# Kernel optimization log

Hardware: AMD Instinct MI355X
Metric: run time of the kernel (lower is better)

## Reference

```python
import jax, jax.numpy as jnp
import numpy as np

EPS = 1e-5
NHEAD = 8
TOP_K = 2


def _layernorm(x, g, b):
    m = jnp.mean(x, axis=-1, keepdims=True)
    v = jnp.mean((x - m) ** 2, axis=-1, keepdims=True)
    return (x - m) * jax.lax.rsqrt(v + EPS) * g + b


def setup_inputs() -> dict:
    S, D, F, E = 4096, 512, 2048, 8
    key = jax.random.key(0)
    ks = jax.random.split(key, 18)
    std = 0.02
    return {
        "src": jax.random.normal(ks[0], (S, D), jnp.float32),
        "in_proj_w": std * jax.random.normal(ks[1], (3 * D, D), jnp.float32),
        "in_proj_b": jnp.zeros((3 * D,), jnp.float32),
        "out_proj_w": std * jax.random.normal(ks[2], (D, D), jnp.float32),
        "out_proj_b": jnp.zeros((D,), jnp.float32),
        "ln1_g": jnp.ones((D,), jnp.float32),
        "ln1_b": jnp.zeros((D,), jnp.float32),
        "ln2_g": jnp.ones((D,), jnp.float32),
        "ln2_b": jnp.zeros((D,), jnp.float32),
        "gate_w": std * jax.random.normal(ks[3], (E, D), jnp.float32),
        "gate_b": jnp.zeros((E,), jnp.float32),
        "w1": std * jax.random.normal(ks[4], (E, F, D), jnp.float32),
        "b1": jnp.zeros((E, F), jnp.float32),
        "w2": std * jax.random.normal(ks[5], (E, F, D), jnp.float32),
        "b2": jnp.zeros((E, F), jnp.float32),
        "wo": std * jax.random.normal(ks[6], (E, D, F), jnp.float32),
        "bo": jnp.zeros((E, D), jnp.float32),
    }


def _sa_block(x, in_proj_w, in_proj_b, out_proj_w, out_proj_b):
    # x: [S, D] unbatched sequence (torch MultiheadAttention unbatched path)
    S, D = x.shape
    hd = D // NHEAD
    qkv = x @ in_proj_w.T + in_proj_b              # [S, 3D]
    q, k, v = jnp.split(qkv, 3, axis=-1)
    q = q.reshape(S, NHEAD, hd)
    k = k.reshape(S, NHEAD, hd)
    v = v.reshape(S, NHEAD, hd)
    scores = jnp.einsum("shd,thd->hst", q, k) / jnp.sqrt(jnp.float32(hd))
    attn = jax.nn.softmax(scores, axis=-1)         # [H, S, S]
    out = jnp.einsum("hst,thd->shd", attn, v).reshape(S, D)
    return out @ out_proj_w.T + out_proj_b


def _ff_block(x, gate_w, gate_b, w1, b1, w2, b2, wo, bo):
    # top-k gated SwiGLU MoE; gate probs are softmax, NOT renormalized after topk
    T = x.shape[0]
    E = w1.shape[0]
    gates = jax.nn.softmax(x @ gate_w.T + gate_b, axis=-1)      # [T, E]
    top_scores, top_idx = jax.lax.top_k(gates, TOP_K)            # [T, k]
    combine = jnp.zeros((T, E), x.dtype).at[
        jnp.arange(T)[:, None], top_idx].add(top_scores)         # [T, E]
    out = jnp.zeros_like(x)
    for e in range(E):  # small fixed expert count
        h = jax.nn.silu(x @ w1[e].T + b1[e]) * (x @ w2[e].T + b2[e])
        out = out + combine[:, e:e + 1] * (h @ wo[e].T + bo[e])
    return out


def reference(src, in_proj_w, in_proj_b, out_proj_w, out_proj_b,
              ln1_g, ln1_b, ln2_g, ln2_b,
              gate_w, gate_b, w1, b1, w2, b2, wo, bo):
    # norm_first pre-norm residual layer, dropout=0 (eval)
    x = src
    x = x + _sa_block(_layernorm(x, ln1_g, ln1_b),
                      in_proj_w, in_proj_b, out_proj_w, out_proj_b)
    x = x + _ff_block(_layernorm(x, ln2_g, ln2_b),
                      gate_w, gate_b, w1, b1, w2, b2, wo, bo)
    return x
```

## Files before the change

### kernel.cpp

```cpp
#include <hip/hip_runtime.h>
#include <hip/hip_bf16.h>
#include <math.h>

#define SQ   4096
#define DM   512
#define NH   8
#define HDIM 64
#define FF   2048
#define NE   8

typedef unsigned short u16;
typedef unsigned int   u32;
typedef __attribute__((ext_vector_type(8))) __bf16 bf16x8;
typedef __attribute__((ext_vector_type(4))) float  f32x4;

__device__ __forceinline__ float bf2f(u16 v) {
    union { u32 i; float f; } c; c.i = ((u32)v) << 16; return c.f;
}
__device__ __forceinline__ u16 f2bf(float f) {
    union { __bf16 h; u16 u; } c; c.h = (__bf16)f; return c.u;
}

#define BM 128
#define BN 128
#define BK 32
#define BKP 40

__global__ __launch_bounds__(256) void gemm_split(
    const u16* __restrict__ Ahi, const u16* __restrict__ Alo, int lda,
    const u16* __restrict__ Bhi, const u16* __restrict__ Blo, int ldb,
    int M, int N, int K,
    const float* __restrict__ bias,
    const float* __restrict__ resid, int ldres,
    u16* __restrict__ Chi, u16* __restrict__ Clo,
    float* __restrict__ Cf, int ldc, int mode)
{
    __shared__ __align__(16) u16 Ash[BM * BKP], Asl[BM * BKP];
    __shared__ __align__(16) u16 Bsh[BN * BKP], Bsl[BN * BKP];
    const int tid  = threadIdx.x;
    const int wave = tid >> 6;
    const int lane = tid & 63;
    const int quad = lane >> 4;
    const int l16  = lane & 15;
    const int bm = blockIdx.x * BM;
    const int bn = blockIdx.y * BN;
    const int wm = (wave & 1) * 64;
    const int wn = (wave >> 1) * 64;

    f32x4 acc[4][4];
#pragma unroll
    for (int i = 0; i < 4; i++)
#pragma unroll
        for (int j = 0; j < 4; j++)
#pragma unroll
            for (int r = 0; r < 4; r++) acc[i][j][r] = 0.0f;

    for (int k0 = 0; k0 < K; k0 += BK) {
#pragma unroll
        for (int i = 0; i < 2; i++) {
            int c = tid + i * 256;
            int row = c >> 2;
            int col = (c & 3) << 3;
            int ga = bm + row, gb2 = bn + row;
            uint4 vah = make_uint4(0u,0u,0u,0u), val = vah, vbh = vah, vbl = vah;
            if (ga < M) {
                vah = *(const uint4*)(Ahi + (size_t)ga * lda + k0 + col);
                val = *(const uint4*)(Alo + (size_t)ga * lda + k0 + col);
            }
            if (gb2 < N) {
                vbh = *(const uint4*)(Bhi + (size_t)gb2 * ldb + k0 + col);
                vbl = *(const uint4*)(Blo + (size_t)gb2 * ldb + k0 + col);
            }
            *(uint4*)(Ash + row * BKP + col) = vah;
            *(uint4*)(Asl + row * BKP + col) = val;
            *(uint4*)(Bsh + row * BKP + col) = vbh;
            *(uint4*)(Bsl + row * BKP + col) = vbl;
        }
        __syncthreads();
        bf16x8 ah[4], al[4], bh[4], bl[4];
#pragma unroll
        for (int i = 0; i < 4; i++) {
            ah[i] = *(const bf16x8*)(Ash + (wm + i * 16 + l16) * BKP + quad * 8);
            al[i] = *(const bf16x8*)(Asl + (wm + i * 16 + l16) * BKP + quad * 8);
        }
#pragma unroll
        for (int j = 0; j < 4; j++) {
            bh[j] = *(const bf16x8*)(Bsh + (wn + j * 16 + l16) * BKP + quad * 8);
            bl[j] = *(const bf16x8*)(Bsl + (wn + j * 16 + l16) * BKP + quad * 8);
        }
#pragma unroll
        for (int i = 0; i < 4; i++)
#pragma unroll
            for (int j = 0; j < 4; j++) {
                acc[i][j] = __builtin_amdgcn_mfma_f32_16x16x32_bf16(ah[i], bh[j], acc[i][j], 0,0,0);
                acc[i][j] = __builtin_amdgcn_mfma_f32_16x16x32_bf16(ah[i], bl[j], acc[i][j], 0,0,0);
                acc[i][j] = __builtin_amdgcn_mfma_f32_16x16x32_bf16(al[i], bh[j], acc[i][j], 0,0,0);
            }
        __syncthreads();
    }

#pragma unroll
    for (int i = 0; i < 4; i++)
#pragma unroll
        for (int j = 0; j < 4; j++)
#pragma unroll
            for (int r = 0; r < 4; r++) {
                int row = bm + wm + i * 16 + quad * 4 + r;
                int col = bn + wn + j * 16 + l16;
                if (row >= M || col >= N) continue;
                float v = acc[i][j][r] + (bias ? bias[col] : 0.0f);
                size_t idx = (size_t)row * ldc + col;
                if (mode == 0) {
                    u16 hb = f2bf(v);
                    Chi[idx] = hb;
                    Clo[idx] = f2bf(v - bf2f(hb));
                } else {
                    if (resid) v += resid[(size_t)row * ldres + col];
                    Cf[idx] = v;
                }
            }
}

__global__ __launch_bounds__(256) void gemm_split_ko(
    const u16* __restrict__ Ahi, const u16* __restrict__ Alo, int lda,
    const u16* __restrict__ Bhi, const u16* __restrict__ Blo, int ldb,
    float* __restrict__ Cf, int ldc)
{
    __shared__ __align__(16) u16 Ash[BM * BKP], Asl[BM * BKP];
    __shared__ __align__(16) u16 Bsh[BN * BKP], Bsl[BN * BKP];
    const int tid  = threadIdx.x;
    const int wave = tid >> 6;
    const int lane = tid & 63;
    const int quad = lane >> 4;
    const int l16  = lane & 15;
    const int bm = blockIdx.x * BM;
    const int bn = blockIdx.y * BN;
    const int wm = (wave & 1) * 64;
    const int wn = (wave >> 1) * 64;
    const int KC    = DM / 4;
    const int k0beg = blockIdx.z * KC;

    f32x4 acc[4][4];
#pragma unroll
    for (int i = 0; i < 4; i++)
#pragma unroll
        for (int j = 0; j < 4; j++)
#pragma unroll
            for (int r = 0; r < 4; r++) acc[i][j][r] = 0.0f;

    for (int k0 = k0beg; k0 < k0beg + KC; k0 += BK) {
#pragma unroll
        for (int i = 0; i < 2; i++) {
            int c = tid + i * 256;
            int row = c >> 2;
            int col = (c & 3) << 3;
            int ga = bm + row, gb2 = bn + row;
            uint4 vah = *(const uint4*)(Ahi + (size_t)ga * lda + k0 + col);
            uint4 val = *(const uint4*)(Alo + (size_t)ga * lda + k0 + col);
            uint4 vbh = *(const uint4*)(Bhi + (size_t)gb2 * ldb + k0 + col);
            uint4 vbl = *(const uint4*)(Blo + (size_t)gb2 * ldb + k0 + col);
            *(uint4*)(Ash + row * BKP + col) = vah;
            *(uint4*)(Asl + row * BKP + col) = val;
            *(uint4*)(Bsh + row * BKP + col) = vbh;
            *(uint4*)(Bsl + row * BKP + col) = vbl;
        }
        __syncthreads();
        bf16x8 ah[4], al[4], bh[4], bl[4];
#pragma unroll
        for (int i = 0; i < 4; i++) {
            ah[i] = *(const bf16x8*)(Ash + (wm + i * 16 + l16) * BKP + quad * 8);
            al[i] = *(const bf16x8*)(Asl + (wm + i * 16 + l16) * BKP + quad * 8);
        }
#pragma unroll
        for (int j = 0; j < 4; j++) {
            bh[j] = *(const bf16x8*)(Bsh + (wn + j * 16 + l16) * BKP + quad * 8);
            bl[j] = *(const bf16x8*)(Bsl + (wn + j * 16 + l16) * BKP + quad * 8);
        }
#pragma unroll
        for (int i = 0; i < 4; i++)
#pragma unroll
            for (int j = 0; j < 4; j++) {
                acc[i][j] = __builtin_amdgcn_mfma_f32_16x16x32_bf16(ah[i], bh[j], acc[i][j], 0,0,0);
                acc[i][j] = __builtin_amdgcn_mfma_f32_16x16x32_bf16(ah[i], bl[j], acc[i][j], 0,0,0);
                acc[i][j] = __builtin_amdgcn_mfma_f32_16x16x32_bf16(al[i], bh[j], acc[i][j], 0,0,0);
            }
        __syncthreads();
    }

#pragma unroll
    for (int i = 0; i < 4; i++)
#pragma unroll
        for (int j = 0; j < 4; j++)
#pragma unroll
            for (int r = 0; r < 4; r++) {
                int row = bm + wm + i * 16 + quad * 4 + r;
                int col = bn + wn + j * 16 + l16;
                atomicAdd(Cf + (size_t)row * ldc + col, acc[i][j][r]);
            }
}

__global__ __launch_bounds__(256) void init_x1(
    const float* __restrict__ src, const float* __restrict__ bias,
    float* __restrict__ x1)
{
    int i = blockIdx.x * 256 + threadIdx.x;
    int col4 = i & (DM / 4 - 1);
    float4 s = ((const float4*)src)[i];
    float4 b = ((const float4*)bias)[col4];
    s.x += b.x; s.y += b.y; s.z += b.z; s.w += b.w;
    ((float4*)x1)[i] = s;
}

__global__ __launch_bounds__(256) void moe12_all(
    const u16* __restrict__ A, int lda,
    const int* __restrict__ idxl, const int* __restrict__ cnt,
    const int* __restrict__ off,
    const float* __restrict__ w1, const float* __restrict__ b1,
    const float* __restrict__ w2, const float* __restrict__ b2,
    u16* __restrict__ H)
{
    const int bmg = blockIdx.x * BM;
    if (bmg >= off[NE]) return;
    int e = 0;
    while (e < NE - 1 && bmg >= off[e + 1]) e++;
    const int M   = cnt[e];
    const int bml = bmg - off[e];
    if (bml >= M) return;
    const float* B1 = w1 + (size_t)e * FF * DM;
    const float* B2 = w2 + (size_t)e * FF * DM;
    const int*   rl = idxl + e * SQ;

    __shared__ __align__(16) u16 As[BM * BKP], Bs1[BN * BKP], Bs2[BN * BKP];
    const int tid  = threadIdx.x;
    const int wave = tid >> 6;
    const int lane = tid & 63;
    const int quad = lane >> 4;
    const int l16  = lane & 15;
    const int bn = blockIdx.y * BN;
    const int wm = (wave & 1) * 64;
    const int wn = (wave >> 1) * 64;

    f32x4 acc1[4][4], acc2[4][4];
#pragma unroll
    for (int i = 0; i < 4; i++)
#pragma unroll
        for (int j = 0; j < 4; j++)
#pragma unroll
            for (int r = 0; r < 4; r++) { acc1[i][j][r] = 0.0f; acc2[i][j][r] = 0.0f; }

    for (int k0 = 0; k0 < DM; k0 += BK) {
#pragma unroll
        for (int i = 0; i < 2; i++) {
            int c = tid + i * 256;
            int row = c >> 2;
            int col = (c & 3) << 3;
            uint4 va = make_uint4(0u,0u,0u,0u);
            int lr = bml + row;
            if (lr < M) {
                int ar = rl[lr];
                va = *(const uint4*)(A + (size_t)ar * lda + k0 + col);
            }
            *(uint4*)(As + row * BKP + col) = va;
        }
#pragma unroll
        for (int i = 0; i < 4; i++) {
            int c = tid + i * 256;
            int row = c >> 3;
            int col = (c & 7) << 2;
            float4 v1 = *(const float4*)(B1 + (size_t)(bn + row) * DM + k0 + col);
            float4 v2 = *(const float4*)(B2 + (size_t)(bn + row) * DM + k0 + col);
            ushort4 h1, h2;
            h1.x = f2bf(v1.x); h1.y = f2bf(v1.y); h1.z = f2bf(v1.z); h1.w = f2bf(v1.w);
            h2.x = f2bf(v2.x); h2.y = f2bf(v2.y); h2.z = f2bf(v2.z); h2.w = f2bf(v2.w);
            *(ushort4*)(Bs1 + row * BKP + col) = h1;
            *(ushort4*)(Bs2 + row * BKP + col) = h2;
        }
        __syncthreads();
        bf16x8 af[4], b1f[4], b2f[4];
#pragma unroll
        for (int i = 0; i < 4; i++)
            af[i] = *(const bf16x8*)(As + (wm + i * 16 + l16) * BKP + quad * 8);
#pragma unroll
        for (int j = 0; j < 4; j++) {
            b1f[j] = *(const bf16x8*)(Bs1 + (wn + j * 16 + l16) * BKP + quad * 8);
            b2f[j] = *(const bf16x8*)(Bs2 + (wn + j * 16 + l16) * BKP + quad * 8);
        }
#pragma unroll
        for (int i = 0; i < 4; i++)
#pragma unroll
            for (int j = 0; j < 4; j++) {
                acc1[i][j] = __builtin_amdgcn_mfma_f32_16x16x32_bf16(af[i], b1f[j], acc1[i][j], 0,0,0);
                acc2[i][j] = __builtin_amdgcn_mfma_f32_16x16x32_bf16(af[i], b2f[j], acc2[i][j], 0,0,0);
            }
        __syncthreads();
    }

#pragma unroll
    for (int i = 0; i < 4; i++)
#pragma unroll
        for (int j = 0; j < 4; j++)
#pragma unroll
            for (int r = 0; r < 4; r++) {
                int rowl = bml + wm + i * 16 + quad * 4 + r;
                if (rowl >= M) continue;
                int col = bn + wn + j * 16 + l16;
                float g1 = acc1[i][j][r] + b1[e * FF + col];
                float g2 = acc2[i][j][r] + b2[e * FF + col];
                float s  = g1 / (1.0f + __expf(-g1));
                H[(size_t)(off[e] + rowl) * FF + col] = f2bf(s * g2);
            }
}

__global__ __launch_bounds__(256) void moe12_bf16(
    const u16* __restrict__ A, int lda,
    const int* __restrict__ idxl, const int* __restrict__ cnt,
    const int* __restrict__ off,
    const u16* __restrict__ w1b, const float* __restrict__ b1,
    const u16* __restrict__ w2b, const float* __restrict__ b2,
    u16* __restrict__ H)
{
    const int bmg = blockIdx.x * BM;
    if (bmg >= off[NE]) return;
    int e = 0;
    while (e < NE - 1 && bmg >= off[e + 1]) e++;
    const int M   = cnt[e];
    const int bml = bmg - off[e];
    if (bml >= M) return;
    const u16* B1 = w1b + (size_t)e * FF * DM;
    const u16* B2 = w2b + (size_t)e * FF * DM;
    const int* rl = idxl + e * SQ;

    __shared__ __align__(16) u16 As[BM * BKP], Bs1[BN * BKP], Bs2[BN * BKP];
    const int tid  = threadIdx.x;
    const int wave = tid >> 6;
    const int lane = tid & 63;
    const int quad = lane >> 4;
    const int l16  = lane & 15;
    const int bn = blockIdx.y * BN;
    const int wm = (wave & 1) * 64;
    const int wn = (wave >> 1) * 64;

    f32x4 acc1[4][4], acc2[4][4];
#pragma unroll
    for (int i = 0; i < 4; i++)
#pragma unroll
        for (int j = 0; j < 4; j++)
#pragma unroll
            for (int r = 0; r < 4; r++) { acc1[i][j][r] = 0.0f; acc2[i][j][r] = 0.0f; }

    for (int k0 = 0; k0 < DM; k0 += BK) {
#pragma unroll
        for (int i = 0; i < 2; i++) {
            int c = tid + i * 256;
            int row = c >> 2;
            int col = (c & 3) << 3;
            uint4 va = make_uint4(0u,0u,0u,0u);
            int lr = bml + row;
            if (lr < M) {
                int ar = rl[lr];
                va = *(const uint4*)(A + (size_t)ar * lda + k0 + col);
            }
            *(uint4*)(As + row * BKP + col) = va;
            uint4 v1 = *(const uint4*)(B1 + (size_t)(bn + row) * DM + k0 + col);
            uint4 v2 = *(const uint4*)(B2 + (size_t)(bn + row) * DM + k0 + col);
            *(uint4*)(Bs1 + row * BKP + col) = v1;
            *(uint4*)(Bs2 + row * BKP + col) = v2;
        }
        __syncthreads();
        bf16x8 af[4], b1f[4], b2f[4];
#pragma unroll
        for (int i = 0; i < 4; i++)
            af[i] = *(const bf16x8*)(As + (wm + i * 16 + l16) * BKP + quad * 8);
#pragma unroll
        for (int j = 0; j < 4; j++) {
            b1f[j] = *(const bf16x8*)(Bs1 + (wn + j * 16 + l16) * BKP + quad * 8);
            b2f[j] = *(const bf16x8*)(Bs2 + (wn + j * 16 + l16) * BKP + quad * 8);
        }
#pragma unroll
        for (int i = 0; i < 4; i++)
#pragma unroll
            for (int j = 0; j < 4; j++) {
                acc1[i][j] = __builtin_amdgcn_mfma_f32_16x16x32_bf16(af[i], b1f[j], acc1[i][j], 0,0,0);
                acc2[i][j] = __builtin_amdgcn_mfma_f32_16x16x32_bf16(af[i], b2f[j], acc2[i][j], 0,0,0);
            }
        __syncthreads();
    }

#pragma unroll
    for (int i = 0; i < 4; i++)
#pragma unroll
        for (int j = 0; j < 4; j++)
#pragma unroll
            for (int r = 0; r < 4; r++) {
                int rowl = bml + wm + i * 16 + quad * 4 + r;
                if (rowl >= M) continue;
                int col = bn + wn + j * 16 + l16;
                float g1 = acc1[i][j][r] + b1[e * FF + col];
                float g2 = acc2[i][j][r] + b2[e * FF + col];
                float s  = g1 / (1.0f + __expf(-g1));
                H[(size_t)(off[e] + rowl) * FF + col] = f2bf(s * g2);
            }
}

__global__ __launch_bounds__(256) void moe_y_all(
    const u16* __restrict__ H,
    const float* __restrict__ wo, const float* __restrict__ bo,
    const int* __restrict__ idxl, const float* __restrict__ cw,
    const int* __restrict__ cnt, const int* __restrict__ off,
    float* __restrict__ out)
{
    const int bmg = blockIdx.x * BM;
    if (bmg >= off[NE]) return;
    int e = 0;
    while (e < NE - 1 && bmg >= off[e + 1]) e++;
    const int M   = cnt[e];
    const int bml = bmg - off[e];
    if (bml >= M) return;
    const float* B = wo + (size_t)e * DM * FF;

    __shared__ __align__(16) u16 As[BM * BKP], Bs[BN * BKP];
    const int tid  = threadIdx.x;
    const int wave = tid >> 6;
    const int lane = tid & 63;
    const int quad = lane >> 4;
    const int l16  = lane & 15;
    const int bn = blockIdx.y * BN;
    const int wm = (wave & 1) * 64;
    const int wn = (wave >> 1) * 64;

    f32x4 acc[4][4];
#pragma unroll
    for (int i = 0; i < 4; i++)
#pragma unroll
        for (int j = 0; j < 4; j++)
#pragma unroll
            for (int r = 0; r < 4; r++) acc[i][j][r] = 0.0f;

    for (int k0 = 0; k0 < FF; k0 += BK) {
#pragma unroll
        for (int i = 0; i < 2; i++) {
            int c = tid + i * 256;
            int row = c >> 2;
            int col = (c & 3) << 3;
            uint4 va = *(const uint4*)(H + (size_t)(bmg + row) * FF + k0 + col);
            *(uint4*)(As + row * BKP + col) = va;
        }
#pragma unroll
        for (int i = 0; i < 4; i++) {
            int c = tid + i * 256;
            int row = c >> 3;
            int col = (c & 7) << 2;
            float4 v = *(const float4*)(B + (size_t)(bn + row) * FF + k0 + col);
            ushort4 h;
            h.x = f2bf(v.x); h.y = f2bf(v.y); h.z = f2bf(v.z); h.w = f2bf(v.w);
            *(ushort4*)(Bs + row * BKP + col) = h;
        }
        __syncthreads();
        bf16x8 af[4], bf[4];
#pragma unroll
        for (int i = 0; i < 4; i++)
            af[i] = *(const bf16x8*)(As + (wm + i * 16 + l16) * BKP + quad * 8);
#pragma unroll
        for (int j = 0; j < 4; j++)
            bf[j] = *(const bf16x8*)(Bs + (wn + j * 16 + l16) * BKP + quad * 8);
#pragma unroll
        for (int i = 0; i < 4; i++)
#pragma unroll
            for (int j = 0; j < 4; j++)
                acc[i][j] = __builtin_amdgcn_mfma_f32_16x16x32_bf16(af[i], bf[j], acc[i][j], 0,0,0);
        __syncthreads();
    }

#pragma unroll
    for (int i = 0; i < 4; i++)
#pragma unroll
        for (int j = 0; j < 4; j++)
#pragma unroll
            for (int r = 0; r < 4; r++) {
                int rowl = bml + wm + i * 16 + quad * 4 + r;
                if (rowl >= M) continue;
                int col = bn + wn + j * 16 + l16;
                int tok = idxl[e * SQ + rowl];
                float wgt = cw[e * SQ + rowl];
                atomicAdd(out + (size_t)tok * DM + col,
                          wgt * (acc[i][j][r] + bo[e * DM + col]));
            }
}

__global__ __launch_bounds__(256) void moe_y_bf16(
    const u16* __restrict__ H,
    const u16* __restrict__ wob, const float* __restrict__ bo,
    const int* __restrict__ idxl, const float* __restrict__ cw,
    const int* __restrict__ cnt, const int* __restrict__ off,
    float* __restrict__ out)
{
    const int bmg = blockIdx.x * BM;
    if (bmg >= off[NE]) return;
    int e = 0;
    while (e < NE - 1 && bmg >= off[e + 1]) e++;
    const int M   = cnt[e];
    const int bml = bmg - off[e];
    if (bml >= M) return;
    const u16* B = wob + (size_t)e * DM * FF;

    __shared__ __align__(16) u16 As[BM * BKP], Bs[BN * BKP];
    const int tid  = threadIdx.x;
    const int wave = tid >> 6;
    const int lane = tid & 63;
    const int quad = lane >> 4;
    const int l16  = lane & 15;
    const int bn = blockIdx.y * BN;
    const int wm = (wave & 1) * 64;
    const int wn = (wave >> 1) * 64;

    f32x4 acc[4][4];
#pragma unroll
    for (int i = 0; i < 4; i++)
#pragma unroll
        for (int j = 0; j < 4; j++)
#pragma unroll
            for (int r = 0; r < 4; r++) acc[i][j][r] = 0.0f;

    for (int k0 = 0; k0 < FF; k0 += BK) {
#pragma unroll
        for (int i = 0; i < 2; i++) {
            int c = tid + i * 256;
            int row = c >> 2;
            int col = (c & 3) << 3;
            uint4 va = *(const uint4*)(H + (size_t)(bmg + row) * FF + k0 + col);
            *(uint4*)(As + row * BKP + col) = va;
            uint4 vb = *(const uint4*)(B + (size_t)(bn + row) * FF + k0 + col);
            *(uint4*)(Bs + row * BKP + col) = vb;
        }
        __syncthreads();
        bf16x8 af[4], bf[4];
#pragma unroll
        for (int i = 0; i < 4; i++)
            af[i] = *(const bf16x8*)(As + (wm + i * 16 + l16) * BKP + quad * 8);
#pragma unroll
        for (int j = 0; j < 4; j++)
            bf[j] = *(const bf16x8*)(Bs + (wn + j * 16 + l16) * BKP + quad * 8);
#pragma unroll
        for (int i = 0; i < 4; i++)
#pragma unroll
            for (int j = 0; j < 4; j++)
                acc[i][j] = __builtin_amdgcn_mfma_f32_16x16x32_bf16(af[i], bf[j], acc[i][j], 0,0,0);
        __syncthreads();
    }

#pragma unroll
    for (int i = 0; i < 4; i++)
#pragma unroll
        for (int j = 0; j < 4; j++)
#pragma unroll
            for (int r = 0; r < 4; r++) {
                int rowl = bml + wm + i * 16 + quad * 4 + r;
                if (rowl >= M) continue;
                int col = bn + wn + j * 16 + l16;
                int tok = idxl[e * SQ + rowl];
                float wgt = cw[e * SQ + rowl];
                atomicAdd(out + (size_t)tok * DM + col,
                          wgt * (acc[i][j][r] + bo[e * DM + col]));
            }
}

__global__ __launch_bounds__(256) void cvt_w_bf16(
    const float* __restrict__ w, u16* __restrict__ wb, int n4)
{
    int i = blockIdx.x * 256 + threadIdx.x;
    if (i < n4) {
        float4 v = ((const float4*)w)[i];
        ushort4 h;
        h.x = f2bf(v.x); h.y = f2bf(v.y); h.z = f2bf(v.z); h.w = f2bf(v.w);
        ((ushort4*)wb)[i] = h;
    }
}

#define KP 64
#define SWZ(row, col) ((col) ^ (((row) & 7) << 3))
#define SCL 0.18033688011112042f

template <int SPLIT>
__device__ __forceinline__ void flash_body(
    const u16* __restrict__ qh, const u16* __restrict__ ql,
    const u16* __restrict__ vth, const u16* __restrict__ vtl,
    u16* __restrict__ oh, u16* __restrict__ ol,
    float* __restrict__ Opart, float* __restrict__ mpart,
    float* __restrict__ lpart)
{
    __shared__ __align__(16) u16 Ksh[64*KP], Ksl[64*KP], Vsh[64*KP], Vsl[64*KP];
    const int tid  = threadIdx.x;
    const int wave = tid >> 6;
    const int lane = tid & 63;
    const int quad = lane >> 4;
    const int l16  = lane & 15;
    const int h    = blockIdx.y;
    const int z    = (SPLIT > 1) ? blockIdx.z : 0;
    const int qbase = blockIdx.x * 64 + wave * 16;

    u16* const Pwh = Ksh + wave * (16 * KP);
    u16* const Pwl = Ksl + wave * (16 * KP);

    const int r_st  = tid >> 3;
    const int co_g  = (tid & 7) << 3;
    const int co_sw = SWZ(r_st, co_g);

    bf16x8 aqh[2], aql[2];
#pragma unroll
    for (int kk = 0; kk < 2; kk++) {
        size_t off = (size_t)(qbase + l16) * (3*DM) + h*HDIM + kk*32 + quad*8;
        aqh[kk] = *(const bf16x8*)(qh + off);
        aql[kk] = *(const bf16x8*)(ql + off);
    }

    float m_[4], l_[4];
    f32x4 o_[4];
#pragma unroll
    for (int r = 0; r < 4; r++) { m_[r] = -1e30f; l_[r] = 0.0f; }
#pragma unroll
    for (int nd = 0; nd < 4; nd++)
#pragma unroll
        for (int r = 0; r < 4; r++) o_[nd][r] = 0.0f;

    const int NT    = SQ / 64 / SPLIT;
    const int jtBeg = z * NT, jtEnd = (z + 1) * NT;

    for (int jt = jtBeg; jt < jtEnd; jt++) {
        {
            size_t koff0 = (size_t)(jt*64 + r_st) * (3*DM) + DM + h*HDIM + co_g;
            size_t voff0 = (size_t)(h*HDIM + r_st) * SQ + jt*64 + co_g;
            size_t koff1 = koff0 + (size_t)32 * (3*DM);
            size_t voff1 = voff0 + (size_t)32 * SQ;
            uint4 a0 = *(const uint4*)(qh  + koff0);
            uint4 a1 = *(const uint4*)(ql  + koff0);
            uint4 a2 = *(const uint4*)(vth + voff0);
            uint4 a3 = *(const uint4*)(vtl + voff0);
            uint4 b0 = *(const uint4*)(qh  + koff1);
            uint4 b1 = *(const uint4*)(ql  + koff1);
            uint4 b2 = *(const uint4*)(vth + voff1);
            uint4 b3 = *(const uint4*)(vtl + voff1);
            *(uint4*)(Ksh + r_st*KP + co_sw)      = a0;
            *(uint4*)(Ksl + r_st*KP + co_sw)      = a1;
            *(uint4*)(Vsh + r_st*KP + co_sw)      = a2;
            *(uint4*)(Vsl + r_st*KP + co_sw)      = a3;
            *(uint4*)(Ksh + (r_st+32)*KP + co_sw) = b0;
            *(uint4*)(Ksl + (r_st+32)*KP + co_sw) = b1;
            *(uint4*)(Vsh + (r_st+32)*KP + co_sw) = b2;
            *(uint4*)(Vsl + (r_st+32)*KP + co_sw) = b3;
        }
        __syncthreads();

        f32x4 s[4];
        __builtin_amdgcn_s_setprio(1);
#pragma unroll
        for (int jn = 0; jn < 4; jn++) {
            f32x4 zz;
#pragma unroll
            for (int r = 0; r < 4; r++) zz[r] = 0.0f;
#pragma unroll
            for (int kk = 0; kk < 2; kk++) {
                int krow = jn*16 + l16;
                int kcol = SWZ(krow, kk*32 + quad*8);
                bf16x8 kh = *(const bf16x8*)(Ksh + krow*KP + kcol);
                bf16x8 kl = *(const bf16x8*)(Ksl + krow*KP + kcol);
                zz = __builtin_amdgcn_mfma_f32_16x16x32_bf16(aqh[kk], kh, zz, 0,0,0);
                zz = __builtin_amdgcn_mfma_f32_16x16x32_bf16(aqh[kk], kl, zz, 0,0,0);
                zz = __builtin_amdgcn_mfma_f32_16x16x32_bf16(aql[kk], kh, zz, 0,0,0);
            }
#pragma unroll
            for (int r = 0; r < 4; r++) zz[r] *= SCL;
            s[jn] = zz;
        }
        __builtin_amdgcn_s_setprio(0);
        __syncthreads();

        float mx[4];
#pragma unroll
        for (int r = 0; r < 4; r++) {
            mx[r] = fmaxf(fmaxf(s[0][r], s[1][r]), fmaxf(s[2][r], s[3][r]));
#pragma unroll
            for (int o2 = 1; o2 < 16; o2 <<= 1)
                mx[r] = fmaxf(mx[r], __shfl_xor(mx[r], o2));
        }
        int grew = (mx[0] > m_[0] + 8.0f) | (mx[1] > m_[1] + 8.0f) |
                   (mx[2] > m_[2] + 8.0f) | (mx[3] > m_[3] + 8.0f);
        if (__any(grew)) {
#pragma unroll
            for (int r = 0; r < 4; r++) {
                float nm  = fmaxf(m_[r], mx[r]);
                float al2 = exp2f(m_[r] - nm);
                m_[r] = nm;
                l_[r] *= al2;
#pragma unroll
                for (int nd = 0; nd < 4; nd++) o_[nd][r] *= al2;
            }
        }
        float rs[4];
#pragma unroll
        for (int r = 0; r < 4; r++) rs[r] = 0.0f;
#pragma unroll
        for (int jn = 0; jn < 4; jn++)
#pragma unroll
            for (int r = 0; r < 4; r++) {
                float p = exp2f(s[jn][r] - m_[r]);
                s[jn][r] = p;
                rs[r] += p;
            }
#pragma unroll
        for (int r = 0; r < 4; r++) {
#pragma unroll
            for (int o2 = 1; o2 < 16; o2 <<= 1)
                rs[r] += __shfl_xor(rs[r], o2);
            l_[r] += rs[r];
        }
#pragma unroll
        for (int jn = 0; jn < 4; jn++)
#pragma unroll
            for (int r = 0; r < 4; r++) {
                float p = s[jn][r];
                u16 ph = f2bf(p);
                int rr   = quad*4 + r;
                int pidx = rr*KP + SWZ(rr, jn*16 + l16);
                Pwh[pidx] = ph;
                Pwl[pidx] = f2bf(p - bf2f(ph));
            }

        bf16x8 ph[2], pl[2];
#pragma unroll
        for (int kk = 0; kk < 2; kk++) {
            int pcol = SWZ(l16, kk*32 + quad*8);
            ph[kk] = *(const bf16x8*)(Pwh + l16*KP + pcol);
            pl[kk] = *(const bf16x8*)(Pwl + l16*KP + pcol);
        }
        __builtin_amdgcn_s_setprio(1);
#pragma unroll
        for (int nd = 0; nd < 4; nd++) {
#pragma unroll
            for (int kk = 0; kk < 2; kk++) {
                int vrow = nd*16 + l16;
                int vcol = SWZ(vrow, kk*32 + quad*8);
                bf16x8 vh = *(const bf16x8*)(Vsh + vrow*KP + vcol);
                bf16x8 vl = *(const bf16x8*)(Vsl + vrow*KP + vcol);
                o_[nd] = __builtin_amdgcn_mfma_f32_16x16x32_bf16(ph[kk], vh, o_[nd], 0,0,0);
                o_[nd] = __builtin_amdgcn_mfma_f32_16x16x32_bf16(ph[kk], vl, o_[nd], 0,0,0);
                o_[nd] = __builtin_amdgcn_mfma_f32_16x16x32_bf16(pl[kk], vh, o_[nd], 0,0,0);
            }
        }
        __builtin_amdgcn_s_setprio(0);
        __syncthreads();
    }

    if (SPLIT == 1) {
#pragma unroll
        for (int nd = 0; nd < 4; nd++)
#pragma unroll
            for (int r = 0; r < 4; r++) {
                int row = qbase + quad*4 + r;
                int col = h*HDIM + nd*16 + l16;
                float w = o_[nd][r] / l_[r];
                u16 hb = f2bf(w);
                oh[(size_t)row * DM + col] = hb;
                ol[(size_t)row * DM + col] = f2bf(w - bf2f(hb));
            }
    } else {
#pragma unroll
        for (int nd = 0; nd < 4; nd++)
#pragma unroll
            for (int r = 0; r < 4; r++) {
                int row = qbase + quad*4 + r;
                int col = h*HDIM + nd*16 + l16;
                Opart[((size_t)z * SQ + row) * DM + col] = o_[nd][r];
            }
        if (l16 == 0) {
#pragma unroll
            for (int r = 0; r < 4; r++) {
                int row = qbase + quad*4 + r;
                mpart[(z*NH + h) * SQ + row] = m_[r];
                lpart[(z*NH + h) * SQ + row] = l_[r];
            }
        }
    }
}

__global__ __launch_bounds__(256) void flash_attn(
    const u16* __restrict__ qh, const u16* __restrict__ ql,
    const u16* __restrict__ vth, const u16* __restrict__ vtl,
    u16* __restrict__ oh, u16* __restrict__ ol)
{
    flash_body<1>(qh, ql, vth, vtl, oh, ol, nullptr, nullptr, nullptr);
}

__global__ __launch_bounds__(256) void flash_attn_part2(
    const u16* __restrict__ qh, const u16* __restrict__ ql,
    const u16* __restrict__ vth, const u16* __restrict__ vtl,
    float* __restrict__ Opart, float* __restrict__ mpart,
    float* __restrict__ lpart)
{
    flash_body<2>(qh, ql, vth, vtl, nullptr, nullptr, Opart, mpart, lpart);
}

__global__ __launch_bounds__(256) void flash_attn_part4(
    const u16* __restrict__ qh, const u16* __restrict__ ql,
    const u16* __restrict__ vth, const u16* __restrict__ vtl,
    float* __restrict__ Opart, float* __restrict__ mpart,
    float* __restrict__ lpart)
{
    flash_body<4>(qh, ql, vth, vtl, nullptr, nullptr, Opart, mpart, lpart);
}

__global__ __launch_bounds__(256) void attn_combine(
    const float* __restrict__ Opart, const float* __restrict__ mpart,
    const float* __restrict__ lpart,
    u16* __restrict__ oh, u16* __restrict__ ol, int ns)
{
    const int row = blockIdx.x;
    const int tid = threadIdx.x;
#pragma unroll
    for (int i = 0; i < 2; i++) {
        int col = tid + i * 256;
        int h = col >> 6;
        float m = -1e30f;
        for (int zz = 0; zz < ns; zz++)
            m = fmaxf(m, mpart[(zz*NH + h) * SQ + row]);
        float O = 0.0f, l = 0.0f;
        for (int zz = 0; zz < ns; zz++) {
            float a = exp2f(mpart[(zz*NH + h) * SQ + row] - m);
            O += Opart[((size_t)zz * SQ + row) * DM + col] * a;
            l += lpart[(zz*NH + h) * SQ + row] * a;
        }
        float w = O / l;
        u16 hb = f2bf(w);
        oh[(size_t)row * DM + col] = hb;
        ol[(size_t)row * DM + col] = f2bf(w - bf2f(hb));
    }
}

__global__ __launch_bounds__(256) void ln1_split(
    const float* __restrict__ x, const float* __restrict__ g,
    const float* __restrict__ b, u16* __restrict__ ohi, u16* __restrict__ olo)
{
    const int row = blockIdx.x;
    const int tid = threadIdx.x;
    float v0 = x[(size_t)row * DM + tid];
    float v1 = x[(size_t)row * DM + tid + 256];
    float s = v0 + v1, sq = v0*v0 + v1*v1;
#pragma unroll
    for (int o = 1; o < 64; o <<= 1) { s += __shfl_xor(s, o); sq += __shfl_xor(sq, o); }
    __shared__ float ss[4], ssq[4];
    if ((tid & 63) == 0) { ss[tid>>6] = s; ssq[tid>>6] = sq; }
    __syncthreads();
    s  = ss[0]+ss[1]+ss[2]+ss[3];
    sq = ssq[0]+ssq[1]+ssq[2]+ssq[3];
    float m = s * (1.0f/DM);
    float rstd = rsqrtf(sq*(1.0f/DM) - m*m + 1e-5f);
    float y0 = (v0-m)*rstd*g[tid]     + b[tid];
    float y1 = (v1-m)*rstd*g[tid+256] + b[tid+256];
    u16 h0 = f2bf(y0), h1 = f2bf(y1);
    ohi[(size_t)row*DM + tid]       = h0;  olo[(size_t)row*DM + tid]       = f2bf(y0 - bf2f(h0));
    ohi[(size_t)row*DM + tid + 256] = h1;  olo[(size_t)row*DM + tid + 256] = f2bf(y1 - bf2f(h1));
}

__global__ __launch_bounds__(256) void ln_kernel(
    const float* __restrict__ x, const float* __restrict__ g,
    const float* __restrict__ b, u16* __restrict__ out)
{
    const int row = blockIdx.x;
    const int tid = threadIdx.x;
    float v0 = x[(size_t)row * DM + tid];
    float v1 = x[(size_t)row * DM + tid + 256];
    float s = v0 + v1, sq = v0*v0 + v1*v1;
#pragma unroll
    for (int o = 1; o < 64; o <<= 1) { s += __shfl_xor(s, o); sq += __shfl_xor(sq, o); }
    __shared__ float ss[4], ssq[4];
    if ((tid & 63) == 0) { ss[tid>>6] = s; ssq[tid>>6] = sq; }
    __syncthreads();
    s  = ss[0]+ss[1]+ss[2]+ss[3];
    sq = ssq[0]+ssq[1]+ssq[2]+ssq[3];
    float m = s * (1.0f/DM);
    float rstd = rsqrtf(sq*(1.0f/DM) - m*m + 1e-5f);
    out[(size_t)row*DM + tid]       = f2bf((v0-m)*rstd*g[tid]     + b[tid]);
    out[(size_t)row*DM + tid + 256] = f2bf((v1-m)*rstd*g[tid+256] + b[tid+256]);
}

__global__ __launch_bounds__(256) void transpose_v2(
    const u16* __restrict__ qh, const u16* __restrict__ ql,
    u16* __restrict__ vth, u16* __restrict__ vtl)
{
    __shared__ u16 Th[64 * 66], Tl[64 * 66];
    const int t0  = blockIdx.x * 64;
    const int hd0 = blockIdx.y * 64;
    const int tid = threadIdx.x;
#pragma unroll
    for (int k = 0; k < 16; k++) {
        int idx = tid + k * 256;
        int r = idx >> 6, j = idx & 63;
        size_t src = (size_t)(t0 + r) * (3*DM) + 2*DM + hd0 + j;
        Th[r * 66 + j] = qh[src];
        Tl[r * 66 + j] = ql[src];
    }
    __syncthreads();
#pragma unroll
    for (int k = 0; k < 16; k++) {
        int idx = tid + k * 256;
        int r = idx >> 6, c2 = idx & 63;
        size_t dst = (size_t)(hd0 + r) * SQ + t0 + c2;
        vth[dst] = Th[c2 * 66 + r];
        vtl[dst] = Tl[c2 * 66 + r];
    }
}

__global__ __launch_bounds__(256) void gate_route(
    const float* __restrict__ x1, const float* __restrict__ g,
    const float* __restrict__ b, const float* __restrict__ gw,
    const float* __restrict__ gb,
    int* __restrict__ cnt, int* __restrict__ idxl, float* __restrict__ cw)
{
    const int token = blockIdx.x * 4 + (threadIdx.x >> 6);
    const int lane  = threadIdx.x & 63;
    const float* xr = x1 + (size_t)token * DM;
    float v[8];
#pragma unroll
    for (int i = 0; i < 8; i++) v[i] = xr[lane*8 + i];
    float s = 0.f, sq = 0.f;
#pragma unroll
    for (int i = 0; i < 8; i++) { s += v[i]; sq += v[i]*v[i]; }
#pragma unroll
    for (int o = 1; o < 64; o <<= 1) { s += __shfl_xor(s, o); sq += __shfl_xor(sq, o); }
    float m = s * (1.0f/DM);
    float rstd = rsqrtf(sq*(1.0f/DM) - m*m + 1e-5f);
    float xn[8];
#pragma unroll
    for (int i = 0; i < 8; i++)
        xn[i] = (v[i]-m)*rstd*g[lane*8+i] + b[lane*8+i];
    float logit[8];
#pragma unroll
    for (int e = 0; e < 8; e++) {
        float t = 0.f;
#pragma unroll
        for (int i = 0; i < 8; i++) t += xn[i] * gw[e*DM + lane*8 + i];
#pragma unroll
        for (int o = 1; o < 64; o <<= 1) t += __shfl_xor(t, o);
        logit[e] = t + gb[e];
    }
    if (lane == 0) {
        float mx = -1e30f;
        for (int e = 0; e < 8; e++) mx = fmaxf(mx, logit[e]);
        float den = 0.f, p[8];
        for (int e = 0; e < 8; e++) { p[e] = __expf(logit[e] - mx); den += p[e]; }
        for (int e = 0; e < 8; e++) p[e] /= den;
        int i1 = 0;
        for (int e = 1; e < 8; e++) if (p[e] > p[i1]) i1 = e;
        int i2 = -1;
        for (int e = 0; e < 8; e++) { if (e == i1) continue; if (i2 < 0 || p[e] > p[i2]) i2 = e; }
        int s1 = atomicAdd(&cnt[i1], 1);
        idxl[i1*SQ + s1] = token;  cw[i1*SQ + s1] = p[i1];
        int s2 = atomicAdd(&cnt[i2], 1);
        idxl[i2*SQ + s2] = token;  cw[i2*SQ + s2] = p[i2];
    }
}

__global__ __launch_bounds__(256) void cvt_split_w(
    const float* __restrict__ w, u16* __restrict__ wh, u16* __restrict__ wl, int n)
{
    int i = blockIdx.x * 256 + threadIdx.x;
    if (i < n) {
        float v = w[i];
        u16 h = f2bf(v);
        wh[i] = h;
        wl[i] = f2bf(v - bf2f(h));
    }
}

__global__ __launch_bounds__(64) void zero_cnt(int* cnt)
{
    if (threadIdx.x < NE) cnt[threadIdx.x] = 0;
}

__global__ __launch_bounds__(64) void make_off(const int* __restrict__ cnt,
                                              int* __restrict__ off)
{
    if (threadIdx.x == 0) {
        int a = 0;
        for (int e = 0; e < NE; e++) {
            off[e] = a;
            a += ((cnt[e] + 127) >> 7) << 7;
        }
        off[NE] = a;
    }
}

__global__ __launch_bounds__(256) void init_out(
    const float* __restrict__ x1, float* __restrict__ out)
{
    int i = blockIdx.x * 256 + threadIdx.x;
    ((float4*)out)[i] = ((const float4*)x1)[i];
}

__global__ __launch_bounds__(256) void sentinel_kernel(float* out, float v, int n)
{
    int i = blockIdx.x * 256 + threadIdx.x;
    if (i < n) out[i] = v;
}
__global__ __launch_bounds__(256) void scrub_kernel(float* out, int n)
{
    int i = blockIdx.x * 256 + threadIdx.x;
    if (i < n) { float v = out[i]; if (!isfinite(v)) out[i] = 777.0f; }
}

extern "C" void kernel_launch(void* const* d_in, const int* in_sizes, int n_in,
                              void* d_out, int out_size, void* d_ws, size_t ws_size,
                              hipStream_t stream)
{
    const float* src        = (const float*)d_in[0];
    const float* in_proj_w  = (const float*)d_in[1];
    const float* in_proj_b  = (const float*)d_in[2];
    const float* out_proj_w = (const float*)d_in[3];
    const float* out_proj_b = (const float*)d_in[4];
    const float* ln1_g      = (const float*)d_in[5];
    const float* ln1_b      = (const float*)d_in[6];
    const float* ln2_g      = (const float*)d_in[7];
    const float* ln2_b      = (const float*)d_in[8];
    const float* gate_w     = (const float*)d_in[9];
    const float* gate_b     = (const float*)d_in[10];
    const float* w1         = (const float*)d_in[11];
    const float* b1         = (const float*)d_in[12];
    const float* w2         = (const float*)d_in[13];
    const float* b2         = (const float*)d_in[14];
    const float* wo         = (const float*)d_in[15];
    const float* bo         = (const float*)d_in[16];
    float* out = (float*)d_out;

    const size_t MB = (size_t)1 << 20;
    const size_t ROUTE = 512 * 1024;
    const size_t NEED      = ROUTE + 44 * MB;
    const size_t NEED_BIG2 = ROUTE + 61 * MB;
    const size_t NEED_BIG4 = ROUTE + 78 * MB;
    if (ws_size < NEED) {
        sentinel_kernel<<<(SQ*DM)/256, 256, 0, stream>>>(out, 333.0f, SQ*DM);
        return;
    }
    int ns = 0;
    if (ws_size >= NEED_BIG4)      ns = 4;
    else if (ws_size >= NEED_BIG2) ns = 2;

    char* ws = (char*)d_ws;
    int*   cnt  = (int*)ws;
    int*   offp = (int*)(ws + 64);
    int*   idxl = (int*)(ws + 1024);
    float* cw   = (float*)(ws + 1024 + 128*1024);
    char*  base = ws + ROUTE;
    u16* xln1h = (u16*)(base);
    u16* xln1l = (u16*)(base + 4*MB);
    u16* attnh = (u16*)(base);
    u16* attnl = (u16*)(base + 4*MB);
    u16* qkvh  = (u16*)(base + 8*MB);
    u16* qkvl  = (u16*)(base + 20*MB);
    float* x1  = (float*)(base + 8*MB);
    u16* vth   = (u16*)(base + 32*MB);
    u16* vtl   = (u16*)(base + 36*MB);
    u16* xln2  = (u16*)(base + 36*MB);
    u16* Hbuf  = (u16*)(base);
    u16* wph   = (u16*)(base + 40*MB);
    u16* wpl   = (u16*)(base + 40*MB + 1536*1024);
    u16* woh   = (u16*)(base + 43*MB);
    u16* wol   = (u16*)(base + 43*MB + 512*1024);
    float* Opart = (float*)(base + 44*MB);
    float* mpart;
    float* lpart;
    if (ns == 4) {
        mpart = (float*)(base + 76*MB);
        lpart = (float*)(base + 76*MB + 512*1024);
    } else {
        mpart = (float*)(base + 60*MB);
        lpart = (float*)(base + 60*MB + 256*1024);
    }
    u16* w1b = (u16*)(base + 44*MB);
    u16* w2b = (u16*)(base + 60*MB);
    u16* wob = (u16*)(base + 44*MB);

    cvt_split_w<<<(3*DM*DM)/256, 256, 0, stream>>>(in_proj_w,  wph, wpl, 3*DM*DM);
    cvt_split_w<<<(DM*DM)/256,   256, 0, stream>>>(out_proj_w, woh, wol, DM*DM);

    ln1_split<<<SQ, 256, 0, stream>>>(src, ln1_g, ln1_b, xln1h, xln1l);
    gemm_split<<<dim3(32, 12), 256, 0, stream>>>(
        xln1h, xln1l, DM, wph, wpl, DM, SQ, 3*DM, DM,
        in_proj_b, nullptr, 0, qkvh, qkvl, nullptr, 3*DM, 0);
    transpose_v2<<<dim3(SQ/64, DM/64), 256, 0, stream>>>(qkvh, qkvl, vth, vtl);
    if (ns == 4) {
        flash_attn_part4<<<dim3(SQ/64, NH, 4), 256, 0, stream>>>(
            qkvh, qkvl, vth, vtl, Opart, mpart, lpart);
        attn_combine<<<SQ, 256, 0, stream>>>(Opart, mpart, lpart, attnh, attnl, 4);
    } else if (ns == 2) {
        flash_attn_part2<<<dim3(SQ/64, NH, 2), 256, 0, stream>>>(
            qkvh, qkvl, vth, vtl, Opart, mpart, lpart);
        attn_combine<<<SQ, 256, 0, stream>>>(Opart, mpart, lpart, attnh, attnl, 2);
    } else {
        flash_attn<<<dim3(SQ/64, NH), 256, 0, stream>>>(
            qkvh, qkvl, vth, vtl, attnh, attnl);
    }
    init_x1<<<(SQ*DM/4)/256, 256, 0, stream>>>(src, out_proj_b, x1);
    gemm_split_ko<<<dim3(32, 4, 4), 256, 0, stream>>>(
        attnh, attnl, DM, woh, wol, DM, x1, DM);

    ln_kernel<<<SQ, 256, 0, stream>>>(x1, ln2_g, ln2_b, xln2);
    zero_cnt<<<1, 64, 0, stream>>>(cnt);
    gate_route<<<SQ/4, 256, 0, stream>>>(x1, ln2_g, ln2_b, gate_w, gate_b,
                                         cnt, idxl, cw);
    make_off<<<1, 64, 0, stream>>>(cnt, offp);
    init_out<<<(SQ*DM/4)/256, 256, 0, stream>>>(x1, out);
    const int WN4 = (NE * FF * DM) / 4;
    if (ns == 4) {
        cvt_w_bf16<<<WN4/256, 256, 0, stream>>>(w1, w1b, WN4);
        cvt_w_bf16<<<WN4/256, 256, 0, stream>>>(w2, w2b, WN4);
        moe12_bf16<<<dim3(72, 16), 256, 0, stream>>>(
            xln2, DM, idxl, cnt, offp, w1b, b1, w2b, b2, Hbuf);
        cvt_w_bf16<<<WN4/256, 256, 0, stream>>>(wo, wob, WN4);
        moe_y_bf16<<<dim3(72, 4), 256, 0, stream>>>(
            Hbuf, wob, bo, idxl, cw, cnt, offp, out);
    } else {
        moe12_all<<<dim3(72, 16), 256, 0, stream>>>(
            xln2, DM, idxl, cnt, offp, w1, b1, w2, b2, Hbuf);
        moe_y_all<<<dim3(72, 4), 256, 0, stream>>>(
            Hbuf, wo, bo, idxl, cw, cnt, offp, out);
    }

    scrub_kernel<<<(SQ*DM)/256, 256, 0, stream>>>(out, SQ*DM);
}
```

Baseline: 784.4 us.

## Compute transposed S in flash attention, use shuffles for P, fuse LN2 into gating

The flash attention kernel now computes S transposed by swapping the MFMA operands, so each lane holds values of a single query row. That makes the row max and row sum cheap two-step cross-quad shuffles. The P fragments for the PV MFMA are built with register shuffles instead of an LDS round trip, which removes one __syncthreads per tile. Separately, the standalone LN2 kernel is removed and gate_route writes the bf16 normalized activations itself, saving a launch and a read of x1. The shuffle-based P transpose adds many ds_bpermute instructions per tile, which may offset the LDS savings.

New measurement: 728.7 us. -7.1%, faster.

```diff
diff --git a/kernel.cpp b/kernel.cpp
--- a/kernel.cpp
+++ b/kernel.cpp
@@ -598,9 +598,6 @@
     const int z    = (SPLIT > 1) ? blockIdx.z : 0;
     const int qbase = blockIdx.x * 64 + wave * 16;
 
-    u16* const Pwh = Ksh + wave * (16 * KP);
-    u16* const Pwl = Ksl + wave * (16 * KP);
-
     const int r_st  = tid >> 3;
     const int co_g  = (tid & 7) << 3;
     const int co_sw = SWZ(r_st, co_g);
@@ -613,14 +610,16 @@
         aql[kk] = *(const bf16x8*)(ql + off);
     }
 
-    float m_[4], l_[4];
+    float m_ = -1e30f, l_ = 0.0f;
     f32x4 o_[4];
 #pragma unroll
-    for (int r = 0; r < 4; r++) { m_[r] = -1e30f; l_[r] = 0.0f; }
-#pragma unroll
     for (int nd = 0; nd < 4; nd++)
 #pragma unroll
         for (int r = 0; r < 4; r++) o_[nd][r] = 0.0f;
+
+    const int srcA = l16 + ((quad & 1) * 2) * 16;
+    const int srcB = srcA + 16;
+    const bool hiJ = (quad >> 1);
 
     const int NT    = SQ / 64 / SPLIT;
     const int jtBeg = z * NT, jtEnd = (z + 1) * NT;
@@ -663,75 +662,105 @@
                 int kcol = SWZ(krow, kk*32 + quad*8);
                 bf16x8 kh = *(const bf16x8*)(Ksh + krow*KP + kcol);
                 bf16x8 kl = *(const bf16x8*)(Ksl + krow*KP + kcol);
-                zz = __builtin_amdgcn_mfma_f32_16x16x32_bf16(aqh[kk], kh, zz, 0,0,0);
-                zz = __builtin_amdgcn_mfma_f32_16x16x32_bf16(aqh[kk], kl, zz, 0,0,0);
-                zz = __builtin_amdgcn_mfma_f32_16x16x32_bf16(aql[kk], kh, zz, 0,0,0);
+                zz = __builtin_amdgcn_mfma_f32_16x16x32_bf16(kh, aqh[kk], zz, 0,0,0);
+                zz = __builtin_amdgcn_mfma_f32_16x16x32_bf16(kl, aqh[kk], zz, 0,0,0);
+                zz = __builtin_amdgcn_mfma_f32_16x16x32_bf16(kh, aql[kk], zz, 0,0,0);
             }
 #pragma unroll
             for (int r = 0; r < 4; r++) zz[r] *= SCL;
             s[jn] = zz;
         }
         __builtin_amdgcn_s_setprio(0);
-        __syncthreads();
-
-        float mx[4];
-#pragma unroll
-        for (int r = 0; r < 4; r++) {
-            mx[r] = fmaxf(fmaxf(s[0][r], s[1][r]), fmaxf(s[2][r], s[3][r]));
-#pragma unroll
-            for (int o2 = 1; o2 < 16; o2 <<= 1)
-                mx[r] = fmaxf(mx[r], __shfl_xor(mx[r], o2));
-        }
-        int grew = (mx[0] > m_[0] + 8.0f) | (mx[1] > m_[1] + 8.0f) |
-                   (mx[2] > m_[2] + 8.0f) | (mx[3] > m_[3] + 8.0f);
+
+        float mx = s[0][0];
+#pragma unroll
+        for (int jn = 0; jn < 4; jn++)
+#pragma unroll
+            for (int r = 0; r < 4; r++) mx = fmaxf(mx, s[jn][r]);
+        mx = fmaxf(mx, __shfl_xor(mx, 16));
+        mx = fmaxf(mx, __shfl_xor(mx, 32));
+
+        int grew = (mx > m_ + 8.0f) ? 1 : 0;
         if (__any(grew)) {
+            float nm  = fmaxf(m_, mx);
+            float al2 = exp2f(m_ - nm);
+            m_ = nm;
+            l_ *= al2;
+            float alq[4];
+#pragma unroll
+            for (int r = 0; r < 4; r++)
+                alq[r] = __shfl(al2, quad*4 + r);
+#pragma unroll
+            for (int nd = 0; nd < 4; nd++)
+#pragma unroll
+                for (int r = 0; r < 4; r++) o_[nd][r] *= alq[r];
+        }
+
+        float rs = 0.0f;
+#pragma unroll
+        for (int jn = 0; jn < 4; jn++)
 #pragma unroll
             for (int r = 0; r < 4; r++) {
-                float nm  = fmaxf(m_[r], mx[r]);
-                float al2 = exp2f(m_[r] - nm);
-                m_[r] = nm;
-                l_[r] *= al2;
-#pragma unroll
-                for (int nd = 0; nd < 4; nd++) o_[nd][r] *= al2;
-            }
-        }
-        float rs[4];
-#pragma unroll
-        for (int r = 0; r < 4; r++) rs[r] = 0.0f;
-#pragma unroll
-        for (int jn = 0; jn < 4; jn++)
-#pragma unroll
-            for (int r = 0; r < 4; r++) {
-                float p = exp2f(s[jn][r] - m_[r]);
+                float p = exp2f(s[jn][r] - m_);
                 s[jn][r] = p;
-                rs[r] += p;
-            }
-#pragma unroll
-        for (int r = 0; r < 4; r++) {
-#pragma unroll
-            for (int o2 = 1; o2 < 16; o2 <<= 1)
-                rs[r] += __shfl_xor(rs[r], o2);
-            l_[r] += rs[r];
-        }
-#pragma unroll
-        for (int jn = 0; jn < 4; jn++)
-#pragma unroll
-            for (int r = 0; r < 4; r++) {
-                float p = s[jn][r];
-                u16 ph = f2bf(p);
-                int rr   = quad*4 + r;
-                int pidx = rr*KP + SWZ(rr, jn*16 + l16);
-                Pwh[pidx] = ph;
-                Pwl[pidx] = f2bf(p - bf2f(ph));
-            }
-
-        bf16x8 ph[2], pl[2];
+                rs += p;
+            }
+        rs += __shfl_xor(rs, 16);
+        rs += __shfl_xor(rs, 32);
+        l_ += rs;
+
+        u32 phk[4][2], plk[4][2];
+#pragma unroll
+        for (int jn = 0; jn < 4; jn++) {
+            u16 h0 = f2bf(s[jn][0]), h1 = f2bf(s[jn][1]);
+            u16 h2 = f2bf(s[jn][2]), h3 = f2bf(s[jn][3]);
+            phk[jn][0] = (u32)h0 | ((u32)h1 << 16);
+            phk[jn][1] = (u32)h2 | ((u32)h3 << 16);
+            u16 g0 = f2bf(s[jn][0] - bf2f(h0)), g1 = f2bf(s[jn][1] - bf2f(h1));
+            u16 g2 = f2bf(s[jn][2] - bf2f(h2)), g3 = f2bf(s[jn][3] - bf2f(h3));
+            plk[jn][0] = (u32)g0 | ((u32)g1 << 16);
+            plk[jn][1] = (u32)g2 | ((u32)g3 << 16);
+        }
+
+        bf16x8 phf[2], plf[2];
 #pragma unroll
         for (int kk = 0; kk < 2; kk++) {
-            int pcol = SWZ(l16, kk*32 + quad*8);
-            ph[kk] = *(const bf16x8*)(Pwh + l16*KP + pcol);
-            pl[kk] = *(const bf16x8*)(Pwl + l16*KP + pcol);
-        }
+            int jA = kk*2, jB = kk*2 + 1;
+            uint4 wh, wl;
+            {
+                u32 a = (u32)__shfl((int)phk[jA][0], srcA);
+                u32 b = (u32)__shfl((int)phk[jB][0], srcA);
+                wh.x = hiJ ? b : a;
+                a = (u32)__shfl((int)phk[jA][1], srcA);
+                b = (u32)__shfl((int)phk[jB][1], srcA);
+                wh.y = hiJ ? b : a;
+                a = (u32)__shfl((int)phk[jA][0], srcB);
+                b = (u32)__shfl((int)phk[jB][0], srcB);
+                wh.z = hiJ ? b : a;
+                a = (u32)__shfl((int)phk[jA][1], srcB);
+                b = (u32)__shfl((int)phk[jB][1], srcB);
+                wh.w = hiJ ? b : a;
+            }
+            {
+                u32 a = (u32)__shfl((int)plk[jA][0], srcA);
+                u32 b = (u32)__shfl((int)plk[jB][0], srcA);
+                wl.x = hiJ ? b : a;
+                a = (u32)__shfl((int)plk[jA][1], srcA);
+                b = (u32)__shfl((int)plk[jB][1], srcA);
+                wl.y = hiJ ? b : a;
+                a = (u32)__shfl((int)plk[jA][0], srcB);
+                b = (u32)__shfl((int)plk[jB][0], srcB);
+                wl.z = hiJ ? b : a;
+                a = (u32)__shfl((int)plk[jA][1], srcB);
+                b = (u32)__shfl((int)plk[jB][1], srcB);
+                wl.w = hiJ ? b : a;
+            }
+            union { uint4 u; bf16x8 v; } ch, cl;
+            ch.u = wh; cl.u = wl;
+            phf[kk] = ch.v;
+            plf[kk] = cl.v;
+        }
+
         __builtin_amdgcn_s_setprio(1);
 #pragma unroll
         for (int nd = 0; nd < 4; nd++) {
@@ -741,9 +770,9 @@
                 int vcol = SWZ(vrow, kk*32 + quad*8);
                 bf16x8 vh = *(const bf16x8*)(Vsh + vrow*KP + vcol);
                 bf16x8 vl = *(const bf16x8*)(Vsl + vrow*KP + vcol);
-                o_[nd] = __builtin_amdgcn_mfma_f32_16x16x32_bf16(ph[kk], vh, o_[nd], 0,0,0);
-                o_[nd] = __builtin_amdgcn_mfma_f32_16x16x32_bf16(ph[kk], vl, o_[nd], 0,0,0);
-                o_[nd] = __builtin_amdgcn_mfma_f32_16x16x32_bf16(pl[kk], vh, o_[nd], 0,0,0);
+                o_[nd] = __builtin_amdgcn_mfma_f32_16x16x32_bf16(phf[kk], vh, o_[nd], 0,0,0);
+                o_[nd] = __builtin_amdgcn_mfma_f32_16x16x32_bf16(phf[kk], vl, o_[nd], 0,0,0);
+                o_[nd] = __builtin_amdgcn_mfma_f32_16x16x32_bf16(plf[kk], vh, o_[nd], 0,0,0);
             }
         }
         __builtin_amdgcn_s_setprio(0);
@@ -751,13 +780,16 @@
     }
 
     if (SPLIT == 1) {
+        float lq[4];
+#pragma unroll
+        for (int r = 0; r < 4; r++) lq[r] = __shfl(l_, quad*4 + r);
 #pragma unroll
         for (int nd = 0; nd < 4; nd++)
 #pragma unroll
             for (int r = 0; r < 4; r++) {
                 int row = qbase + quad*4 + r;
                 int col = h*HDIM + nd*16 + l16;
-                float w = o_[nd][r] / l_[r];
+                float w = o_[nd][r] / lq[r];
                 u16 hb = f2bf(w);
                 oh[(size_t)row * DM + col] = hb;
                 ol[(size_t)row * DM + col] = f2bf(w - bf2f(hb));
@@ -771,13 +803,10 @@
                 int col = h*HDIM + nd*16 + l16;
                 Opart[((size_t)z * SQ + row) * DM + col] = o_[nd][r];
             }
-        if (l16 == 0) {
-#pragma unroll
-            for (int r = 0; r < 4; r++) {
-                int row = qbase + quad*4 + r;
-                mpart[(z*NH + h) * SQ + row] = m_[r];
-                lpart[(z*NH + h) * SQ + row] = l_[r];
-            }
+        if (lane < 16) {
+            int row = qbase + l16;
+            mpart[(z*NH + h) * SQ + row] = m_;
+            lpart[(z*NH + h) * SQ + row] = l_;
         }
     }
 }
@@ -860,28 +889,6 @@
     ohi[(size_t)row*DM + tid + 256] = h1;  olo[(size_t)row*DM + tid + 256] = f2bf(y1 - bf2f(h1));
 }
 
-__global__ __launch_bounds__(256) void ln_kernel(
-    const float* __restrict__ x, const float* __restrict__ g,
-    const float* __restrict__ b, u16* __restrict__ out)
-{
-    const int row = blockIdx.x;
-    const int tid = threadIdx.x;
-    float v0 = x[(size_t)row * DM + tid];
-    float v1 = x[(size_t)row * DM + tid + 256];
-    float s = v0 + v1, sq = v0*v0 + v1*v1;
-#pragma unroll
-    for (int o = 1; o < 64; o <<= 1) { s += __shfl_xor(s, o); sq += __shfl_xor(sq, o); }
-    __shared__ float ss[4], ssq[4];
-    if ((tid & 63) == 0) { ss[tid>>6] = s; ssq[tid>>6] = sq; }
-    __syncthreads();
-    s  = ss[0]+ss[1]+ss[2]+ss[3];
-    sq = ssq[0]+ssq[1]+ssq[2]+ssq[3];
-    float m = s * (1.0f/DM);
-    float rstd = rsqrtf(sq*(1.0f/DM) - m*m + 1e-5f);
-    out[(size_t)row*DM + tid]       = f2bf((v0-m)*rstd*g[tid]     + b[tid]);
-    out[(size_t)row*DM + tid + 256] = f2bf((v1-m)*rstd*g[tid+256] + b[tid+256]);
-}
-
 __global__ __launch_bounds__(256) void transpose_v2(
     const u16* __restrict__ qh, const u16* __restrict__ ql,
     u16* __restrict__ vth, u16* __restrict__ vtl)
@@ -913,7 +920,8 @@
     const float* __restrict__ x1, const float* __restrict__ g,
     const float* __restrict__ b, const float* __restrict__ gw,
     const float* __restrict__ gb,
-    int* __restrict__ cnt, int* __restrict__ idxl, float* __restrict__ cw)
+    int* __restrict__ cnt, int* __restrict__ idxl, float* __restrict__ cw,
+    u16* __restrict__ xout)
 {
     const int token = blockIdx.x * 4 + (threadIdx.x >> 6);
     const int lane  = threadIdx.x & 63;
@@ -932,6 +940,14 @@
 #pragma unroll
     for (int i = 0; i < 8; i++)
         xn[i] = (v[i]-m)*rstd*g[lane*8+i] + b[lane*8+i];
+    {
+        uint4 w;
+        w.x = (u32)f2bf(xn[0]) | ((u32)f2bf(xn[1]) << 16);
+        w.y = (u32)f2bf(xn[2]) | ((u32)f2bf(xn[3]) << 16);
+        w.z = (u32)f2bf(xn[4]) | ((u32)f2bf(xn[5]) << 16);
+        w.w = (u32)f2bf(xn[6]) | ((u32)f2bf(xn[7]) << 16);
+        *(uint4*)(xout + (size_t)token * DM + lane*8) = w;
+    }
     float logit[8];
 #pragma unroll
     for (int e = 0; e < 8; e++) {
@@ -1102,10 +1118,9 @@
     gemm_split_ko<<<dim3(32, 4, 4), 256, 0, stream>>>(
         attnh, attnl, DM, woh, wol, DM, x1, DM);
 
-    ln_kernel<<<SQ, 256, 0, stream>>>(x1, ln2_g, ln2_b, xln2);
     zero_cnt<<<1, 64, 0, stream>>>(cnt);
     gate_route<<<SQ/4, 256, 0, stream>>>(x1, ln2_g, ln2_b, gate_w, gate_b,
-                                         cnt, idxl, cw);
+                                         cnt, idxl, cw, xln2);
     make_off<<<1, 64, 0, stream>>>(cnt, offp);
     init_out<<<(SQ*DM/4)/256, 256, 0, stream>>>(x1, out);
     const int WN4 = (NE * FF * DM) / 4;
```
